# Kernel optimization log

Hardware: AMD Instinct MI355X
Metric: run time of the kernel (lower is better)

## Reference

```python
import jax, jax.numpy as jnp
import numpy as np
import math

B, T, C = 4, 2048, 1024
NH, D = 16, 64


def setup_inputs() -> dict:
    key = jax.random.key(0)
    ks = jax.random.split(key, 7)
    s = 0.02
    return {
        "x": jax.random.normal(ks[0], (B, T, C), dtype=jnp.float32),
        "W_attn": jax.random.normal(ks[1], (C, 3 * C), dtype=jnp.float32) * s,
        "b_attn": jax.random.normal(ks[2], (3 * C,), dtype=jnp.float32) * s,
        "W_proj": jax.random.normal(ks[3], (C, C), dtype=jnp.float32) * s,
        "b_proj": jax.random.normal(ks[4], (C,), dtype=jnp.float32) * s,
        # bQ/bK emulate mean_Q + std_Q*randn (resampled biases), broadcast over heads
        "bQ": 0.5 + 0.1 * jax.random.normal(ks[5], (NH, D), dtype=jnp.float32),
        "bK": 0.3 + 0.1 * jax.random.normal(ks[6], (NH, D), dtype=jnp.float32),
    }


def reference(x, W_attn, b_attn, W_proj, b_proj, bQ, bK):
    b, t, c = x.shape
    nh, d = bQ.shape
    qkv = x @ W_attn + b_attn                       # [B,T,3C]
    q, k, v = jnp.split(qkv, 3, axis=2)
    # [B,T,C] -> [B,nh,T,d]
    q = q.reshape(b, t, nh, d).transpose(0, 2, 1, 3)
    k = k.reshape(b, t, nh, d).transpose(0, 2, 1, 3)
    v = v.reshape(b, t, nh, d).transpose(0, 2, 1, 3)
    q = q + bQ[None, :, None, :]
    k = k + bK[None, :, None, :]
    scores = jnp.einsum('bhqd,bhkd->bhqk', q, k) / math.sqrt(d)
    causal = jnp.tril(jnp.ones((t, t), dtype=bool))
    scores = jnp.where(causal[None, None], scores, jnp.finfo(scores.dtype).min)
    att = jax.nn.softmax(scores, axis=-1)
    y = jnp.einsum('bhqk,bhkd->bhqd', att, v)       # [B,nh,T,d]
    y = y.transpose(0, 2, 1, 3).reshape(b, t, c)
    out = y @ W_proj + b_proj
    return (out, bQ)
```

## Files before the change

kernel.cpp:

```cpp
#include <hip/hip_runtime.h>
#include <hip/hip_bf16.h>

#define B_  4
#define T_  2048
#define C_  1024
#define NH_ 16
#define D_  64
#define BH_ (B_*NH_)
#define M_  (B_*T_)

typedef __attribute__((ext_vector_type(8))) short short8;
typedef __attribute__((ext_vector_type(4))) short short4v;
typedef __attribute__((ext_vector_type(4))) float f32x4;

#define SC2 0.18033688011112043f

__device__ __forceinline__ ushort f2bf(float f) {
    unsigned u = __float_as_uint(f);
    u += 0x7FFF + ((u >> 16) & 1);
    return (ushort)(u >> 16);
}

__device__ __forceinline__ unsigned cvtpk(float lo, float hi) {
    unsigned r;
    asm("v_cvt_pk_bf16_f32 %0, %1, %2" : "=v"(r) : "v"(lo), "v"(hi));
    return r;
}

__device__ __forceinline__ void gload16(const void* g, void* lds) {
    __builtin_amdgcn_global_load_lds(
        (const __attribute__((address_space(1))) void*)g,
        (__attribute__((address_space(3))) void*)lds, 16, 0, 0);
}

__global__ __launch_bounds__(256) void prepass_kernel(
    const float* __restrict__ x, ushort* __restrict__ Xb,
    const float* __restrict__ Wa, ushort* __restrict__ Wat,
    const float* __restrict__ bQ, float* __restrict__ bqDst)
{
    __shared__ float t[64][65];
    const int bid = blockIdx.x;
    const int tid = threadIdx.x;

    if (bid < 2048) {
        const int n8 = M_*C_/8;
        const int stride = 2048 * 256;
        for (int idx = bid*256 + tid; idx < n8; idx += stride) {
            const float* p = x + (size_t)idx * 8;
            f32x4 a = *(const f32x4*)p;
            f32x4 b = *(const f32x4*)(p + 4);
            union { short8 v; ushort u[8]; } pk;
            #pragma unroll
            for (int j = 0; j < 4; ++j) { pk.u[j] = f2bf(a[j]); pk.u[4+j] = f2bf(b[j]); }
            *(short8*)&Xb[(size_t)idx * 8] = pk.v;
        }
    } else if (bid < 2816) {
        const int tb = bid - 2048;
        const int n0 = (tb % 48) * 64;
        const int k0 = (tb / 48) * 64;
        const int K = C_, N = 3*C_;
        #pragma unroll
        for (int it = 0; it < 16; ++it) {
            const int kr = it*4 + (tid >> 6);
            t[kr][tid & 63] = Wa[(size_t)(k0 + kr) * N + n0 + (tid & 63)];
        }
        __syncthreads();
        const int nr8 = tid >> 3;
        const int kc0 = (tid & 7) * 8;
        #pragma unroll
        for (int j = 0; j < 2; ++j) {
            const int nr = j*32 + nr8;
            union { short8 v; ushort u[8]; } pk;
            #pragma unroll
            for (int e = 0; e < 8; ++e) pk.u[e] = f2bf(t[kc0 + e][nr]);
            *(short8*)&Wat[(size_t)(n0 + nr) * K + k0 + kc0] = pk.v;
        }
    } else {
        for (int i = tid; i < NH_*D_; i += 256) bqDst[i] = bQ[i];
    }
}

__global__ __launch_bounds__(256) void transpose_w_kernel(
    const float* __restrict__ in, ushort* __restrict__ out, int K, int N)
{
    __shared__ float t[64][65];
    const int tid = threadIdx.x;
    const int n0 = blockIdx.x * 64;
    const int k0 = blockIdx.y * 64;
    #pragma unroll
    for (int it = 0; it < 16; ++it) {
        const int kr = it*4 + (tid >> 6);
        t[kr][tid & 63] = in[(size_t)(k0 + kr) * N + n0 + (tid & 63)];
    }
    __syncthreads();
    const int nr8 = tid >> 3;
    const int kc0 = (tid & 7) * 8;
    #pragma unroll
    for (int j = 0; j < 2; ++j) {
        const int nr = j*32 + nr8;
        union { short8 v; ushort u[8]; } pk;
        #pragma unroll
        for (int e = 0; e < 8; ++e) pk.u[e] = f2bf(t[kc0 + e][nr]);
        *(short8*)&out[(size_t)(n0 + nr) * K + k0 + kc0] = pk.v;
    }
}

__global__ __launch_bounds__(512, 2) void gemmqkv_kernel(
    const ushort* __restrict__ A, const ushort* __restrict__ Bt,
    const float* __restrict__ b_attn, const float* __restrict__ bQv,
    const float* __restrict__ bKv,
    ushort* __restrict__ Qb, ushort* __restrict__ Kb, ushort* __restrict__ Vt)
{
    __shared__ ushort SH[65536];

    const int K = C_;
    const int NT = 16;
    const int tid  = threadIdx.x;
    const int lane = tid & 63;
    const int w    = tid >> 6;
    const int wr   = w >> 2;
    const int wc   = w & 3;
    const int l16  = lane & 15, lg = lane >> 4;

    const int bid = blockIdx.x;
    const int xcd = bid & 7;
    const int idx = bid >> 3;
    const int m0  = (xcd*4 + (idx & 3)) * 256;
    const int n0  = (idx >> 2) * 256;

    const int gsw = 8 * ((lane & 3) ^ ((lane >> 3) & 3));
    const ushort* aBase = A  + (size_t)(m0 + w*32 + (lane >> 2)) * K + gsw;
    const ushort* bBase = Bt + (size_t)(n0 + w*32 + (lane >> 2)) * K + gsw;
    const int fsw = ((lg ^ ((l16 >> 1) & 3)) << 3);

    f32x4 acc[8][4] = {};

    #define STG_A(tk, kh)                                                     \
        do { ushort* d_ = SH + ((tk)&1)*16384 + (kh)*8192 + w*1024;           \
             const ushort* s_ = aBase + (tk)*64 + (kh)*32;                    \
             gload16(s_, d_); gload16(s_ + 16*K, d_ + 512); } while (0)
    #define STG_B(tk, kh)                                                     \
        do { ushort* d_ = SH + 32768 + ((tk)&1)*16384 + (kh)*8192 + w*1024;   \
             const ushort* s_ = bBase + (tk)*64 + (kh)*32;                    \
             gload16(s_, d_); gload16(s_ + 16*K, d_ + 512); } while (0)
    #define BAR()   __builtin_amdgcn_s_barrier()
    #define LGKM()  do { asm volatile("s_waitcnt lgkmcnt(0)" ::: "memory");   \
                         __builtin_amdgcn_sched_barrier(0); } while (0)
    #define VMC4()  asm volatile("s_waitcnt vmcnt(4)" ::: "memory")
    #define VMC0()  asm volatile("s_waitcnt vmcnt(0)" ::: "memory")

    STG_A(0, 0); STG_B(0, 0); STG_A(0, 1); STG_B(0, 1);
    VMC4();
    BAR();

    #pragma unroll 1
    for (int t = 0; t < NT; ++t) {
        const int cb = (t & 1) * 16384;
        const bool st = (t + 1 < NT);
        short8 bf[4], af[4];

        {
            const ushort* Ah = SH + cb;
            const ushort* Bh = SH + 32768 + cb;
            #pragma unroll
            for (int ni = 0; ni < 4; ++ni)
                bf[ni] = *(const short8*)&Bh[(wc*64 + ni*16 + l16)*32 + fsw];
            #pragma unroll
            for (int q = 0; q < 4; ++q)
                af[q] = *(const short8*)&Ah[(wr*128 + q*16 + l16)*32 + fsw];
            if (st) STG_A(t + 1, 0);
            BAR(); LGKM();
            __builtin_amdgcn_s_setprio(1);
            #pragma unroll
            for (int q = 0; q < 4; ++q)
                #pragma unroll
                for (int ni = 0; ni < 4; ++ni)
                    acc[q][ni] = __builtin_amdgcn_mfma_f32_16x16x32_bf16(
                        af[q], bf[ni], acc[q][ni], 0, 0, 0);
            __builtin_amdgcn_s_setprio(0);
            BAR();
        }
        {
            const ushort* Ah = SH + cb;
            #pragma unroll
            for (int q = 0; q < 4; ++q)
                af[q] = *(const short8*)&Ah[(wr*128 + (4+q)*16 + l16)*32 + fsw];
            if (st) STG_B(t + 1, 0);
            BAR(); LGKM();
            __builtin_amdgcn_s_setprio(1);
            #pragma unroll
            for (int q = 0; q < 4; ++q)
                #pragma unroll
                for (int ni = 0; ni < 4; ++ni)
                    acc[4+q][ni] = __builtin_amdgcn_mfma_f32_16x16x32_bf16(
                        af[q], bf[ni], acc[4+q][ni], 0, 0, 0);
            __builtin_amdgcn_s_setprio(0);
            if (st) VMC4(); else VMC0();
            BAR();
        }
        {
            const ushort* Ah = SH + cb + 8192;
            const ushort* Bh = SH + 32768 + cb + 8192;
            #pragma unroll
            for (int ni = 0; ni < 4; ++ni)
                bf[ni] = *(const short8*)&Bh[(wc*64 + ni*16 + l16)*32 + fsw];
            #pragma unroll
            for (int q = 0; q < 4; ++q)
                af[q] = *(const short8*)&Ah[(wr*128 + q*16 + l16)*32 + fsw];
            if (st) STG_A(t + 1, 1);
            BAR(); LGKM();
            __builtin_amdgcn_s_setprio(1);
            #pragma unroll
            for (int q = 0; q < 4; ++q)
                #pragma unroll
                for (int ni = 0; ni < 4; ++ni)
                    acc[q][ni] = __builtin_amdgcn_mfma_f32_16x16x32_bf16(
                        af[q], bf[ni], acc[q][ni], 0, 0, 0);
            __builtin_amdgcn_s_setprio(0);
            BAR();
        }
        {
            const ushort* Ah = SH + cb + 8192;
            #pragma unroll
            for (int q = 0; q < 4; ++q)
                af[q] = *(const short8*)&Ah[(wr*128 + (4+q)*16 + l16)*32 + fsw];
            if (st) STG_B(t + 1, 1);
            BAR(); LGKM();
            __builtin_amdgcn_s_setprio(1);
            #pragma unroll
            for (int q = 0; q < 4; ++q)
                #pragma unroll
                for (int ni = 0; ni < 4; ++ni)
                    acc[4+q][ni] = __builtin_amdgcn_mfma_f32_16x16x32_bf16(
                        af[q], bf[ni], acc[4+q][ni], 0, 0, 0);
            __builtin_amdgcn_s_setprio(0);
            if (st) VMC4();
            BAR();
        }
    }
    #undef STG_A
    #undef STG_B

    if (n0 < 2048) {
        #pragma unroll
        for (int ni = 0; ni < 4; ++ni) {
            const int n = n0 + wc*64 + ni*16 + l16;
            const int sec = n >> 10;
            const int nn  = n & 1023;
            const int h = nn >> 6, d = nn & 63;
            const float ba = b_attn[n];
            #pragma unroll
            for (int mi = 0; mi < 8; ++mi) {
                #pragma unroll
                for (int r = 0; r < 4; ++r) {
                    const int m = m0 + wr*128 + mi*16 + lg*4 + r;
                    const int b = m >> 11, tt = m & 2047;
                    float v = acc[mi][ni][r] + ba;
                    if (sec == 0) {
                        v = (v + bQv[nn]) * SC2;
                        Qb[((size_t)(b*NH_ + h)*T_ + tt)*D_ + d] = f2bf(v);
                    } else {
                        v += bKv[nn];
                        Kb[((size_t)(b*NH_ + h)*T_ + tt)*D_ + d] = f2bf(v);
                    }
                }
            }
        }
    } else {
        ushort* TL = SH;
        const int bblk = m0 >> 11;
        const int tcol0 = m0 & 2047;
        const int h0 = (n0 & 1023) >> 6;
        #pragma unroll 1
        for (int mh = 0; mh < 2; ++mh) {
            __syncthreads();
            if (wr == mh) {
                #pragma unroll
                for (int ni = 0; ni < 4; ++ni) {
                    const int nl = wc*64 + ni*16 + l16;
                    const float ba = b_attn[n0 + nl];
                    #pragma unroll
                    for (int mi = 0; mi < 8; ++mi)
                        #pragma unroll
                        for (int r = 0; r < 4; ++r)
                            TL[nl*132 + mi*16 + lg*4 + r] =
                                f2bf(acc[mi][ni][r] + ba);
                }
            }
            __syncthreads();
            #pragma unroll
            for (int it = 0; it < 8; ++it) {
                const int row = w*32 + it*4 + lg;
                const int d = row & 63;
                const int h = h0 + (row >> 6);
                const short8 v = *(const short8*)&TL[row*132 + l16*8];
                *(short8*)(Vt + ((size_t)(bblk*NH_ + h)*D_ + d)*T_
                           + tcol0 + mh*128 + l16*8) = v;
            }
        }
    }
}

__global__ __launch_bounds__(256) void gemm2_kernel(
    const ushort* __restrict__ A, const ushort* __restrict__ Bt,
    float* __restrict__ outp, const float* __restrict__ b_proj,
    int K, int N)
{
    __shared__ ushort SH[24576];

    const int tid  = threadIdx.x;
    const int lane = tid & 63;
    const int w    = tid >> 6;
    const int wr   = w >> 1, wc = w & 1;
    const int l16  = lane & 15, lg = lane >> 4;

    const int bid = blockIdx.x;
    const int xcd = bid & 7;
    const int idx = bid >> 3;
    const int m0  = (xcd*8 + (idx & 7)) * 128;
    const int n0  = (idx >> 3) * 128;

    const int srow = lane >> 2;
    const int scol = (lane & 3) * 8;
    const ushort* aS = A  + (size_t)(m0 + w*32 + srow) * K + scol;
    const ushort* bS = Bt + (size_t)(n0 + w*32 + srow) * K + scol;

    f32x4 acc[4][4] = {};
    const int NT = K >> 5;

    #define STAGE(tk, bi)                                                     \
        do {                                                                  \
            const int kn_ = (tk) * 32;                                        \
            gload16(aS + kn_,                SH + (bi)*4096 + w*1024);        \
            gload16(aS + (size_t)16*K + kn_, SH + (bi)*4096 + w*1024 + 512);  \
            gload16(bS + kn_,                SH + 12288 + (bi)*4096 + w*1024);\
            gload16(bS + (size_t)16*K + kn_, SH + 12288 + (bi)*4096 + w*1024 + 512);\
        } while (0)

    STAGE(0, 0);
    STAGE(1, 1);
    asm volatile("s_waitcnt vmcnt(4)" ::: "memory");
    __builtin_amdgcn_s_barrier();

    for (int t = 0; t < NT; ++t) {
        const int cur = t % 3;
        if (t + 2 < NT)
            STAGE(t + 2, (t + 2) % 3);

        short8 af[4], bf[4];
        #pragma unroll
        for (int i = 0; i < 4; ++i) {
            af[i] = *(const short8*)&SH[cur*4096 + (wr*64 + i*16 + l16)*32 + lg*8];
            bf[i] = *(const short8*)&SH[12288 + cur*4096 + (wc*64 + i*16 + l16)*32 + lg*8];
        }
        #pragma unroll
        for (int mi = 0; mi < 4; ++mi)
            #pragma unroll
            for (int ni = 0; ni < 4; ++ni)
                acc[mi][ni] = __builtin_amdgcn_mfma_f32_16x16x32_bf16(
                    af[mi], bf[ni], acc[mi][ni], 0, 0, 0);

        if (t + 1 < NT) {
            if (t + 2 < NT)
                asm volatile("s_waitcnt vmcnt(4)" ::: "memory");
            else
                asm volatile("s_waitcnt vmcnt(0)" ::: "memory");
            __builtin_amdgcn_s_barrier();
        }
    }
    #undef STAGE

    #pragma unroll
    for (int ni = 0; ni < 4; ++ni) {
        const int n = n0 + wc*64 + ni*16 + l16;
        const float bp = b_proj[n];
        #pragma unroll
        for (int mi = 0; mi < 4; ++mi)
            #pragma unroll
            for (int r = 0; r < 4; ++r) {
                const int m = m0 + wr*64 + mi*16 + lg*4 + r;
                outp[(size_t)m * N + n] = acc[mi][ni][r] + bp;
            }
    }
}

__global__ __launch_bounds__(256, 5) void attn_kernel(
    const ushort* __restrict__ Qb, const ushort* __restrict__ Kb,
    const ushort* __restrict__ Vt, ushort* __restrict__ y)
{
    __shared__ char lds[2][16384];

    const int tid  = threadIdx.x;
    const int lane = tid & 63;
    const int w    = tid >> 6;
    const int l16  = lane & 15, lg = lane >> 4;
    const int bid  = blockIdx.x;
    const int xcd  = bid & 7;
    const int idx  = bid >> 3;
    const int bh   = (xcd << 3) | (idx & 7);
    const int p    = 31 - (idx >> 3);
    const int b    = bh >> 4, h = bh & 15;
    const size_t kvb = (size_t)bh * T_ * D_;
    const size_t vtb = (size_t)bh * D_ * T_;

    int srow[2], scol[2];
    #pragma unroll
    for (int i = 0; i < 2; ++i) {
        const int l = w*2048 + i*1024 + lane*16;
        const int r = l >> 7;
        const int c = (l & 127) ^ ((r & 7) << 4);
        srow[i] = r; scol[i] = c >> 1;
    }

    const f32x4 z4 = {0.f, 0.f, 0.f, 0.f};

    const int qw = p * 64 + w * 16;

    short8 qf[2];
    #pragma unroll
    for (int c = 0; c < 2; ++c)
        qf[c] = *(const short8*)(Qb + kvb +
                    (size_t)(qw + l16)*D_ + c*32 + lg*8);

    f32x4 o[4] = {};
    float mrow = -1e30f;
    float lrow = 0.f;
    const int nt = p + 1;

    #pragma unroll
    for (int i = 0; i < 2; ++i) {
        gload16(Kb + kvb + (size_t)srow[i]*D_ + scol[i],
                &lds[0][w*2048 + i*1024]);
        gload16(Vt + vtb + (size_t)srow[i]*T_ + scol[i],
                &lds[0][8192 + w*2048 + i*1024]);
    }

    #pragma unroll 1
    for (int t = 0; t < nt; ++t) {
        const int kb = t * 64;
        if (t + 1 < nt) {
            char* Lb = lds[(t + 1) & 1];
            const int kb1 = kb + 64;
            #pragma unroll
            for (int i = 0; i < 2; ++i) {
                gload16(Kb + kvb + (size_t)(kb1 + srow[i])*D_ + scol[i],
                        Lb + w*2048 + i*1024);
                gload16(Vt + vtb + (size_t)srow[i]*T_ + kb1 + scol[i],
                        Lb + 8192 + w*2048 + i*1024);
            }
            asm volatile("s_waitcnt vmcnt(4)" ::: "memory");
        } else {
            asm volatile("s_waitcnt vmcnt(0)" ::: "memory");
        }
        __builtin_amdgcn_s_barrier();

        {
            const char* Lk = lds[t & 1];
            const char* Lv = lds[t & 1] + 8192;

            f32x4 s[4];
            #pragma unroll
            for (int t4 = 0; t4 < 4; ++t4) {
                const int r = t4*16 + l16;
                const int m = (r & 7) << 4;
                const short8 kc0 = *(const short8*)(Lk + r*128 + (( lg*16     ) ^ m));
                const short8 kc1 = *(const short8*)(Lk + r*128 + ((64 + lg*16 ) ^ m));
                s[t4] = __builtin_amdgcn_mfma_f32_16x16x32_bf16(kc0, qf[0], z4,    0, 0, 0);
                s[t4] = __builtin_amdgcn_mfma_f32_16x16x32_bf16(kc1, qf[1], s[t4], 0, 0, 0);
            }

            const bool full = (kb + 63 <= qw);
            float x[4][4];
            #pragma unroll
            for (int t4 = 0; t4 < 4; ++t4)
                #pragma unroll
                for (int r = 0; r < 4; ++r) {
                    float v = s[t4][r];
                    if (!full)
                        v = (kb + t4*16 + lg*4 + r <= qw + l16) ? v : -1e30f;
                    x[t4][r] = v;
                }
            float vm0 = fmaxf(fmaxf(x[0][0], x[0][1]), fmaxf(x[0][2], x[0][3]));
            float vm1 = fmaxf(fmaxf(x[1][0], x[1][1]), fmaxf(x[1][2], x[1][3]));
            float vm2 = fmaxf(fmaxf(x[2][0], x[2][1]), fmaxf(x[2][2], x[2][3]));
            float vm3 = fmaxf(fmaxf(x[3][0], x[3][1]), fmaxf(x[3][2], x[3][3]));
            float vm  = fmaxf(fmaxf(vm0, vm1), fmaxf(vm2, vm3));
            vm = fmaxf(vm, __shfl_xor(vm, 16, 64));
            vm = fmaxf(vm, __shfl_xor(vm, 32, 64));
            const float mn = fmaxf(mrow, vm);
            float rs = 0.f;
            #pragma unroll
            for (int t4 = 0; t4 < 4; ++t4)
                #pragma unroll
                for (int r = 0; r < 4; ++r) {
                    const float pe = __builtin_amdgcn_exp2f(x[t4][r] - mn);
                    x[t4][r] = pe;
                    rs += pe;
                }
            rs += __shfl_xor(rs, 16, 64);
            rs += __shfl_xor(rs, 32, 64);
            if (__all(vm <= mrow)) {
                lrow += rs;
            } else {
                const float al = __builtin_amdgcn_exp2f(mrow - mn);
                lrow = lrow*al + rs;
                #pragma unroll
                for (int cb = 0; cb < 4; ++cb)
                    #pragma unroll
                    for (int r = 0; r < 4; ++r)
                        o[cb][r] *= al;
            }
            mrow = mn;

            union { unsigned u[4]; short8 v; } p0, p1;
            p0.u[0] = cvtpk(x[0][0], x[0][1]);
            p0.u[1] = cvtpk(x[0][2], x[0][3]);
            p0.u[2] = cvtpk(x[1][0], x[1][1]);
            p0.u[3] = cvtpk(x[1][2], x[1][3]);
            p1.u[0] = cvtpk(x[2][0], x[2][1]);
            p1.u[1] = cvtpk(x[2][2], x[2][3]);
            p1.u[2] = cvtpk(x[3][0], x[3][1]);
            p1.u[3] = cvtpk(x[3][2], x[3][3]);

            #pragma unroll
            for (int cb = 0; cb < 4; ++cb) {
                const int d = cb*16 + l16;
                const int mv = (d & 7) << 4;
                const char* vb = Lv + d*128;
                union { short8 v; short4v hh[2]; } v0, v1;
                v0.hh[0] = *(const short4v*)(vb + ((lg*8     ) ^ mv));
                v0.hh[1] = *(const short4v*)(vb + ((lg*8 + 32) ^ mv));
                v1.hh[0] = *(const short4v*)(vb + ((lg*8 + 64) ^ mv));
                v1.hh[1] = *(const short4v*)(vb + ((lg*8 + 96) ^ mv));
                o[cb] = __builtin_amdgcn_mfma_f32_16x16x32_bf16(v0.v, p0.v, o[cb], 0, 0, 0);
                o[cb] = __builtin_amdgcn_mfma_f32_16x16x32_bf16(v1.v, p1.v, o[cb], 0, 0, 0);
            }
        }
        __builtin_amdgcn_s_barrier();
    }

    {
        const float inv = 1.0f / lrow;
        const int q = qw + l16;
        ushort* yr = y + ((size_t)b*T_ + q)*C_ + h*D_ + lg*4;
        #pragma unroll
        for (int cb = 0; cb < 4; ++cb) {
            union { unsigned u[2]; short4v v; } st;
            st.u[0] = cvtpk(o[cb][0]*inv, o[cb][1]*inv);
            st.u[1] = cvtpk(o[cb][2]*inv, o[cb][3]*inv);
            *(short4v*)(yr + cb*16) = st.v;
        }
    }
}

extern "C" void kernel_launch(void* const* d_in, const int* in_sizes, int n_in,
                              void* d_out, int out_size, void* d_ws, size_t ws_size,
                              hipStream_t stream)
{
    const float* x      = (const float*)d_in[0];
    const float* W_attn = (const float*)d_in[1];
    const float* b_attn = (const float*)d_in[2];
    const float* W_proj = (const float*)d_in[3];
    const float* b_proj = (const float*)d_in[4];
    const float* bQ     = (const float*)d_in[5];
    const float* bK     = (const float*)d_in[6];
    float* out = (float*)d_out;

    const size_t HE = (size_t)BH_ * T_ * D_;
    ushort* Qb = (ushort*)d_ws;
    ushort* Kb = Qb + HE;
    ushort* Vt = Kb + HE;
    ushort* y  = Vt + HE;
    ushort* Wpt = (ushort*)d_ws;

    ushort* Xb  = (ushort*)d_out;
    ushort* Wat = (ushort*)d_out + (size_t)M_ * C_;

    prepass_kernel<<<2817, 256, 0, stream>>>(x, Xb, W_attn, Wat,
                                             bQ, out + (size_t)M_ * C_);

    gemmqkv_kernel<<<384, 512, 0, stream>>>(
        Xb, Wat, b_attn, bQ, bK, Qb, Kb, Vt);

    attn_kernel<<<2048, 256, 0, stream>>>(Qb, Kb, Vt, y);

    transpose_w_kernel<<<dim3(C_/64, C_/64), 256, 0, stream>>>(W_proj, Wpt, C_, C_);

    gemm2_kernel<<<512, 256, 0, stream>>>(
        y, Wpt, out, b_proj, C_, C_);
}
```

Measured before the change: 197.1 us.

## Switch QKV GEMM to a 4-stage LDS ring with one barrier per step

After: 197.8 us. No clear change (+0.4%).

```diff
diff --git a/kernel.cpp b/kernel.cpp
--- a/kernel.cpp
+++ b/kernel.cpp
@@ -114,7 +114,7 @@
     __shared__ ushort SH[65536];
 
     const int K = C_;
-    const int NT = 16;
+    const int NT = 32;
     const int tid  = threadIdx.x;
     const int lane = tid & 63;
     const int w    = tid >> 6;
@@ -128,118 +128,79 @@
     const int m0  = (xcd*4 + (idx & 3)) * 256;
     const int n0  = (idx >> 2) * 256;
 
-    const int gsw = 8 * ((lane & 3) ^ ((lane >> 3) & 3));
-    const ushort* aBase = A  + (size_t)(m0 + w*32 + (lane >> 2)) * K + gsw;
-    const ushort* bBase = Bt + (size_t)(n0 + w*32 + (lane >> 2)) * K + gsw;
-    const int fsw = ((lg ^ ((l16 >> 1) & 3)) << 3);
+    const ushort* aBase = A  + (size_t)(m0 + w*32 + (lane >> 2)) * K + (lane & 3)*8;
+    const ushort* bBase = Bt + (size_t)(n0 + w*32 + (lane >> 2)) * K + (lane & 3)*8;
 
     f32x4 acc[8][4] = {};
 
-    #define STG_A(tk, kh)                                                     \
-        do { ushort* d_ = SH + ((tk)&1)*16384 + (kh)*8192 + w*1024;           \
-             const ushort* s_ = aBase + (tk)*64 + (kh)*32;                    \
-             gload16(s_, d_); gload16(s_ + 16*K, d_ + 512); } while (0)
-    #define STG_B(tk, kh)                                                     \
-        do { ushort* d_ = SH + 32768 + ((tk)&1)*16384 + (kh)*8192 + w*1024;   \
-             const ushort* s_ = bBase + (tk)*64 + (kh)*32;                    \
-             gload16(s_, d_); gload16(s_ + 16*K, d_ + 512); } while (0)
-    #define BAR()   __builtin_amdgcn_s_barrier()
+    #define STG_A(tk)                                                         \
+        do { ushort* d_ = SH + ((tk)&3)*8192 + w*1024;                        \
+             const ushort* s_ = aBase + (size_t)(tk)*32;                      \
+             gload16(s_, d_); gload16(s_ + (size_t)16*K, d_ + 512); } while (0)
+    #define STG_B(tk)                                                         \
+        do { ushort* d_ = SH + 32768 + ((tk)&3)*8192 + w*1024;                \
+             const ushort* s_ = bBase + (size_t)(tk)*32;                      \
+             gload16(s_, d_); gload16(s_ + (size_t)16*K, d_ + 512); } while (0)
     #define LGKM()  do { asm volatile("s_waitcnt lgkmcnt(0)" ::: "memory");   \
                          __builtin_amdgcn_sched_barrier(0); } while (0)
-    #define VMC4()  asm volatile("s_waitcnt vmcnt(4)" ::: "memory")
-    #define VMC0()  asm volatile("s_waitcnt vmcnt(0)" ::: "memory")
-
-    STG_A(0, 0); STG_B(0, 0); STG_A(0, 1); STG_B(0, 1);
-    VMC4();
-    BAR();
+
+    STG_A(0); STG_B(0);
+    STG_A(1); STG_B(1);
+    STG_A(2); STG_B(2);
+    asm volatile("s_waitcnt vmcnt(8)" ::: "memory");
+    __builtin_amdgcn_s_barrier();
 
     #pragma unroll 1
     for (int t = 0; t < NT; ++t) {
-        const int cb = (t & 1) * 16384;
-        const bool st = (t + 1 < NT);
-        short8 bf[4], af[4];
-
-        {
-            const ushort* Ah = SH + cb;
-            const ushort* Bh = SH + 32768 + cb;
+        const ushort* Ab = SH + (t & 3)*8192;
+        const ushort* Bb = SH + 32768 + (t & 3)*8192;
+        const bool st = (t + 3 < NT);
+        short8 af[4], bf[4];
+
+        #pragma unroll
+        for (int ni = 0; ni < 4; ++ni)
+            bf[ni] = *(const short8*)&Bb[(wc*64 + ni*16 + l16)*32 + lg*8];
+        #pragma unroll
+        for (int i = 0; i < 4; ++i)
+            af[i] = *(const short8*)&Ab[(wr*128 + i*16 + l16)*32 + lg*8];
+        if (st) STG_A(t + 3);
+        LGKM();
+        __builtin_amdgcn_s_setprio(1);
+        #pragma unroll
+        for (int i = 0; i < 4; ++i)
             #pragma unroll
             for (int ni = 0; ni < 4; ++ni)
-                bf[ni] = *(const short8*)&Bh[(wc*64 + ni*16 + l16)*32 + fsw];
-            #pragma unroll
-            for (int q = 0; q < 4; ++q)
-                af[q] = *(const short8*)&Ah[(wr*128 + q*16 + l16)*32 + fsw];
-            if (st) STG_A(t + 1, 0);
-            BAR(); LGKM();
-            __builtin_amdgcn_s_setprio(1);
-            #pragma unroll
-            for (int q = 0; q < 4; ++q)
-                #pragma unroll
-                for (int ni = 0; ni < 4; ++ni)
-                    acc[q][ni] = __builtin_amdgcn_mfma_f32_16x16x32_bf16(
-                        af[q], bf[ni], acc[q][ni], 0, 0, 0);
-            __builtin_amdgcn_s_setprio(0);
-            BAR();
-        }
-        {
-            const ushort* Ah = SH + cb;
-            #pragma unroll
-            for (int q = 0; q < 4; ++q)
-                af[q] = *(const short8*)&Ah[(wr*128 + (4+q)*16 + l16)*32 + fsw];
-            if (st) STG_B(t + 1, 0);
-            BAR(); LGKM();
-            __builtin_amdgcn_s_setprio(1);
-            #pragma unroll
-            for (int q = 0; q < 4; ++q)
-                #pragma unroll
-                for (int ni = 0; ni < 4; ++ni)
-                    acc[4+q][ni] = __builtin_amdgcn_mfma_f32_16x16x32_bf16(
-                        af[q], bf[ni], acc[4+q][ni], 0, 0, 0);
-            __builtin_amdgcn_s_setprio(0);
-            if (st) VMC4(); else VMC0();
-            BAR();
-        }
-        {
-            const ushort* Ah = SH + cb + 8192;
-            const ushort* Bh = SH + 32768 + cb + 8192;
+                acc[i][ni] = __builtin_amdgcn_mfma_f32_16x16x32_bf16(
+                    af[i], bf[ni], acc[i][ni], 0, 0, 0);
+        __builtin_amdgcn_s_setprio(0);
+
+        #pragma unroll
+        for (int i = 0; i < 4; ++i)
+            af[i] = *(const short8*)&Ab[(wr*128 + (4+i)*16 + l16)*32 + lg*8];
+        if (st) STG_B(t + 3);
+        LGKM();
+        __builtin_amdgcn_s_setprio(1);
+        #pragma unroll
+        for (int i = 0; i < 4; ++i)
             #pragma unroll
             for (int ni = 0; ni < 4; ++ni)
-                bf[ni] = *(const short8*)&Bh[(wc*64 + ni*16 + l16)*32 + fsw];
-            #pragma unroll
-            for (int q = 0; q < 4; ++q)
-                af[q] = *(const short8*)&Ah[(wr*128 + q*16 + l16)*32 + fsw];
-            if (st) STG_A(t + 1, 1);
-            BAR(); LGKM();
-            __builtin_amdgcn_s_setprio(1);
-            #pragma unroll
-            for (int q = 0; q < 4; ++q)
-                #pragma unroll
-                for (int ni = 0; ni < 4; ++ni)
-                    acc[q][ni] = __builtin_amdgcn_mfma_f32_16x16x32_bf16(
-                        af[q], bf[ni], acc[q][ni], 0, 0, 0);
-            __builtin_amdgcn_s_setprio(0);
-            BAR();
-        }
-        {
-            const ushort* Ah = SH + cb + 8192;
-            #pragma unroll
-            for (int q = 0; q < 4; ++q)
-                af[q] = *(const short8*)&Ah[(wr*128 + (4+q)*16 + l16)*32 + fsw];
-            if (st) STG_B(t + 1, 1);
-            BAR(); LGKM();
-            __builtin_amdgcn_s_setprio(1);
-            #pragma unroll
-            for (int q = 0; q < 4; ++q)
-                #pragma unroll
-                for (int ni = 0; ni < 4; ++ni)
-                    acc[4+q][ni] = __builtin_amdgcn_mfma_f32_16x16x32_bf16(
-                        af[q], bf[ni], acc[4+q][ni], 0, 0, 0);
-            __builtin_amdgcn_s_setprio(0);
-            if (st) VMC4();
-            BAR();
+                acc[4+i][ni] = __builtin_amdgcn_mfma_f32_16x16x32_bf16(
+                    af[i], bf[ni], acc[4+i][ni], 0, 0, 0);
+        __builtin_amdgcn_s_setprio(0);
+
+        if (t + 1 < NT) {
+            if (t + 3 < NT)
+                asm volatile("s_waitcnt vmcnt(8)" ::: "memory");
+            else if (t + 2 < NT)
+                asm volatile("s_waitcnt vmcnt(4)" ::: "memory");
+            else
+                asm volatile("s_waitcnt vmcnt(0)" ::: "memory");
+            __builtin_amdgcn_s_barrier();
         }
     }
     #undef STG_A
     #undef STG_B
+    #undef LGKM
 
     if (n0 < 2048) {
         #pragma unroll
```
